# Kernel optimization log

Measured on AMD Instinct MI355X. Metric: run time of the kernel, lower is better.

The kernel has to match this reference:

```python
import jax, jax.numpy as jnp
import numpy as np

N, L, D = 16, 3136, 768  # batch, H*W (perfect square: 56*56), hidden_size
H = 8                    # head_count
K = D                    # key_channels
V = D // 2               # value_channels
M = 4 * D                # mlp_dim
EPS = 1e-6


def setup_inputs() -> dict:
    key = jax.random.key(0)
    ks = jax.random.split(key, 12)
    s = lambda d: 1.0 / np.sqrt(d)
    return {
        "x": jax.random.normal(ks[0], (N, L, D), dtype=jnp.float32),
        "ln1_g": jnp.ones((D,), jnp.float32),
        "ln1_b": jnp.zeros((D,), jnp.float32),
        # 1x1 conv weights stored as [out_ch, in_ch]
        "Wk": jax.random.normal(ks[1], (K, D), jnp.float32) * s(D),
        "bk": jnp.zeros((K,), jnp.float32),
        "Wq": jax.random.normal(ks[2], (K, D), jnp.float32) * s(D),
        "bq": jnp.zeros((K,), jnp.float32),
        "Wv": jax.random.normal(ks[3], (V, D), jnp.float32) * s(D),
        "bv": jnp.zeros((V,), jnp.float32),
        "Wr": jax.random.normal(ks[4], (D, V), jnp.float32) * s(V),
        "br": jnp.zeros((D,), jnp.float32),
        "ln2_g": jnp.ones((D,), jnp.float32),
        "ln2_b": jnp.zeros((D,), jnp.float32),
        # Linear weights stored as [out, in] (torch convention)
        "W1": jax.random.normal(ks[5], (M, D), jnp.float32) * s(D),
        "b1": jax.random.normal(ks[6], (M,), jnp.float32) * 1e-6,
        "W2": jax.random.normal(ks[7], (D, M), jnp.float32) * s(M),
        "b2": jax.random.normal(ks[8], (D,), jnp.float32) * 1e-6,
    }


def _layernorm(x, g, b):
    m = jnp.mean(x, axis=-1, keepdims=True)
    v = jnp.mean(jnp.square(x - m), axis=-1, keepdims=True)
    return (x - m) * jax.lax.rsqrt(v + EPS) * g + b


def _efficient_attention(x, Wk, bk, Wq, bq, Wv, bv, Wr, br):
    n, l, d = x.shape
    hk, hv = K // H, V // H
    # faithful to torch: input_.view(n, D, h, w) is a raw reshape, not transpose
    xf = x.reshape(n, d, l)  # [n, D, L]
    keys = jnp.einsum('kd,ndl->nkl', Wk, xf) + bk[None, :, None]
    queries = jnp.einsum('kd,ndl->nkl', Wq, xf) + bq[None, :, None]
    values = jnp.einsum('vd,ndl->nvl', Wv, xf) + bv[None, :, None]
    kh = jax.nn.softmax(keys.reshape(n, H, hk, l), axis=3)     # softmax over spatial
    qh = jax.nn.softmax(queries.reshape(n, H, hk, l), axis=2)  # softmax over head channels
    vh = values.reshape(n, H, hv, l)
    context = jnp.einsum('nhkl,nhvl->nhkv', kh, vh)            # [n,H,hk,hv]
    att = jnp.einsum('nhkv,nhkl->nhvl', context, qh)           # [n,H,hv,L]
    agg = att.reshape(n, V, l)
    out = jnp.einsum('dv,nvl->ndl', Wr, agg) + br[None, :, None]
    return out.reshape(n, l, d)  # faithful raw reshape back


def reference(x, ln1_g, ln1_b, Wk, bk, Wq, bq, Wv, bv, Wr, br,
              ln2_g, ln2_b, W1, b1, W2, b2):
    h = x
    y = _layernorm(x, ln1_g, ln1_b)
    y = _efficient_attention(y, Wk, bk, Wq, bq, Wv, bv, Wr, br)
    x = y + h
    h = x
    y = _layernorm(x, ln2_g, ln2_b)
    y = jax.nn.gelu(y @ W1.T + b1, approximate=False)
    y = y @ W2.T + b2
    return y + h
```

## Files before the change

### kernel.cpp

```cpp
#include <hip/hip_runtime.h>
#include <hip/hip_bf16.h>

using bf16 = __hip_bfloat16;
typedef __attribute__((ext_vector_type(8))) short short8;
typedef __attribute__((ext_vector_type(4))) short short4v;
typedef __attribute__((ext_vector_type(4))) float f32x4;

__device__ __forceinline__ float bfbits2f(unsigned short h) {
    unsigned v = (unsigned)h << 16;
    return __uint_as_float(v);
}

__device__ __forceinline__ void gload16(const void* g, void* l) {
    __builtin_amdgcn_global_load_lds(
        (const __attribute__((address_space(1))) unsigned int*)g,
        (__attribute__((address_space(3))) unsigned int*)l, 16, 0, 0);
}

__device__ __forceinline__ float gelu_fast(float x) {
    float x2 = x * x;
    float u = x * __builtin_fmaf(0.07135481f, x2, 1.59576912f);
    float e = __expf(u);
    return x - x * __builtin_amdgcn_rcpf(e + 1.0f);
}

__device__ __forceinline__ float blk_sum3(float v, float* red) {
#pragma unroll
    for (int o = 32; o > 0; o >>= 1) v += __shfl_down(v, o, 64);
    int wv = threadIdx.x >> 6;
    __syncthreads();
    if ((threadIdx.x & 63) == 0) red[wv] = v;
    __syncthreads();
    return red[0] + red[1] + red[2];
}

__global__ __launch_bounds__(192) void ln_f32(const float* __restrict__ x,
                                              const float* __restrict__ g,
                                              const float* __restrict__ b,
                                              bf16* __restrict__ y) {
    __shared__ float red[3];
    size_t base = (size_t)blockIdx.x * 768;
    int t = threadIdx.x;
    float4 v = *(const float4*)&x[base + t * 4];
    float s = blk_sum3(v.x + v.y + v.z + v.w, red);
    float mean = s * (1.0f / 768.0f);
    float d0 = v.x - mean, d1 = v.y - mean, d2 = v.z - mean, d3 = v.w - mean;
    float sq = blk_sum3(d0 * d0 + d1 * d1 + d2 * d2 + d3 * d3, red);
    float rstd = rsqrtf(sq * (1.0f / 768.0f) + 1e-6f);
    float4 gv = *(const float4*)&g[t * 4];
    float4 bv = *(const float4*)&b[t * 4];
    short4v o;
    o[0] = (short)__bfloat16_as_ushort(__float2bfloat16(d0 * rstd * gv.x + bv.x));
    o[1] = (short)__bfloat16_as_ushort(__float2bfloat16(d1 * rstd * gv.y + bv.y));
    o[2] = (short)__bfloat16_as_ushort(__float2bfloat16(d2 * rstd * gv.z + bv.z));
    o[3] = (short)__bfloat16_as_ushort(__float2bfloat16(d3 * rstd * gv.w + bv.w));
    *(short4v*)&((unsigned short*)y)[base + t * 4] = o;
}

__global__ __launch_bounds__(192) void ln_bf(const bf16* __restrict__ x,
                                             const float* __restrict__ g,
                                             const float* __restrict__ b,
                                             bf16* __restrict__ y) {
    __shared__ float red[3];
    size_t base = (size_t)blockIdx.x * 768;
    int t = threadIdx.x;
    short4v w = *(const short4v*)&((const unsigned short*)x)[base + t * 4];
    float v0 = bfbits2f((unsigned short)w[0]), v1 = bfbits2f((unsigned short)w[1]);
    float v2 = bfbits2f((unsigned short)w[2]), v3 = bfbits2f((unsigned short)w[3]);
    float s = blk_sum3(v0 + v1 + v2 + v3, red);
    float mean = s * (1.0f / 768.0f);
    float d0 = v0 - mean, d1 = v1 - mean, d2 = v2 - mean, d3 = v3 - mean;
    float sq = blk_sum3(d0 * d0 + d1 * d1 + d2 * d2 + d3 * d3, red);
    float rstd = rsqrtf(sq * (1.0f / 768.0f) + 1e-6f);
    float4 gv = *(const float4*)&g[t * 4];
    float4 bv = *(const float4*)&b[t * 4];
    short4v o;
    o[0] = (short)__bfloat16_as_ushort(__float2bfloat16(d0 * rstd * gv.x + bv.x));
    o[1] = (short)__bfloat16_as_ushort(__float2bfloat16(d1 * rstd * gv.y + bv.y));
    o[2] = (short)__bfloat16_as_ushort(__float2bfloat16(d2 * rstd * gv.z + bv.z));
    o[3] = (short)__bfloat16_as_ushort(__float2bfloat16(d3 * rstd * gv.w + bv.w));
    *(short4v*)&((unsigned short*)y)[base + t * 4] = o;
}

__global__ __launch_bounds__(256) void cast_kernel(const float* __restrict__ s,
                                                   bf16* __restrict__ d, int n) {
    int i = blockIdx.x * 256 + threadIdx.x;
    if (i < n) d[i] = __float2bfloat16(s[i]);
}

__global__ __launch_bounds__(256) void bias_cat(const float* __restrict__ bk,
                                                const float* __restrict__ bq,
                                                const float* __restrict__ bv,
                                                float* __restrict__ o) {
    int i = blockIdx.x * 256 + threadIdx.x;
    if (i < 768) o[i] = bk[i];
    else if (i < 1536) o[i] = bq[i - 768];
    else if (i < 1920) o[i] = bv[i - 1536];
}

__global__ __launch_bounds__(256) void transp_k(const bf16* __restrict__ Y,
                                                bf16* __restrict__ Xt) {
    __shared__ unsigned short tile[64][65];
    const size_t LD = (size_t)768 * 3136;
    int n = blockIdx.z;
    int l0 = blockIdx.x * 64, d0 = blockIdx.y * 64;
    const unsigned short* Yp = (const unsigned short*)Y + (size_t)n * LD;
    unsigned short* Xp = (unsigned short*)Xt + (size_t)n * LD;
    int t = threadIdx.x;
#pragma unroll
    for (int j = 0; j < 2; j++) {
        int e = t + 256 * j;
        int dd = e >> 3, lg = (e & 7) * 8;
        short8 v = *(const short8*)&Yp[(size_t)(d0 + dd) * 3136 + l0 + lg];
#pragma unroll
        for (int u = 0; u < 8; u++) tile[dd][lg + u] = (unsigned short)v[u];
    }
    __syncthreads();
#pragma unroll
    for (int j = 0; j < 2; j++) {
        int e = t + 256 * j;
        int ll = e >> 3, dg = (e & 7) * 8;
        short8 v;
#pragma unroll
        for (int u = 0; u < 8; u++) v[u] = (short)tile[dg + u][ll];
        *(short8*)&Xp[(size_t)(l0 + ll) * 768 + d0 + dg] = v;
    }
}

template <int MODE>
__global__ __launch_bounds__(256) void gemm_nk(
    const bf16* __restrict__ A, const bf16* __restrict__ B,
    const float* __restrict__ bias, const void* __restrict__ resid,
    void* __restrict__ C0, void* __restrict__ C1, void* __restrict__ C2,
    int M, int N, int K, long sB, long sC, long sR) {
    __shared__ bf16 As[128 * 64];
    __shared__ bf16 Bs[128 * 64];
    const int tid = threadIdx.x;
    const int lane = tid & 63, wave = tid >> 6;

    const int nbn = gridDim.x;
    const int nwg = nbn * gridDim.y;
    const int orig = blockIdx.y * nbn + blockIdx.x;
    const int qq = nwg >> 3, rm = nwg & 7;
    const int xcd = orig & 7, pos = orig >> 3;
    const int work = (xcd < rm ? xcd * (qq + 1) : rm * (qq + 1) + (xcd - rm) * qq) + pos;
    const int bn = work % nbn, bm = work / nbn;
    const int bz = blockIdx.z;

    const int wm = (wave >> 1) * 64, wn = (wave & 1) * 64;
    const int frow = lane & 15, fsb = lane >> 4;
    const int fxr = frow & 7;

    const int srow = lane >> 3;
    const int sslot = (lane & 7) ^ srow;
    const size_t rowB = (size_t)K * 2;
    const char* Ap = (const char*)A +
        ((size_t)bm * 128 + wave * 32 + srow) * rowB + (size_t)sslot * 16;
    const char* Bp = (const char*)(B + (size_t)bz * sB) +
        ((size_t)bn * 128 + wave * 32 + srow) * rowB + (size_t)sslot * 16;

    f32x4 acc[4][4];
#pragma unroll
    for (int mi = 0; mi < 4; mi++)
#pragma unroll
        for (int ni = 0; ni < 4; ni++)
#pragma unroll
            for (int r = 0; r < 4; r++) acc[mi][ni][r] = 0.0f;

    for (int kt = 0; kt < K; kt += 64) {
#pragma unroll
        for (int c = 0; c < 4; c++) {
            gload16(Ap + (size_t)c * 8 * rowB + (size_t)kt * 2, &As[(wave * 4 + c) * 512]);
            gload16(Bp + (size_t)c * 8 * rowB + (size_t)kt * 2, &Bs[(wave * 4 + c) * 512]);
        }
        __syncthreads();
#pragma unroll
        for (int k2 = 0; k2 < 2; k2++) {
            short8 af[4], bfv[4];
#pragma unroll
            for (int mi = 0; mi < 4; mi++) {
                int r = wm + mi * 16 + frow;
                af[mi] = *(const short8*)&As[r * 64 + (((k2 * 4 + fsb) ^ fxr) << 3)];
            }
#pragma unroll
            for (int ni = 0; ni < 4; ni++) {
                int r = wn + ni * 16 + frow;
                bfv[ni] = *(const short8*)&Bs[r * 64 + (((k2 * 4 + fsb) ^ fxr) << 3)];
            }
#pragma unroll
            for (int mi = 0; mi < 4; mi++)
#pragma unroll
                for (int ni = 0; ni < 4; ni++)
                    acc[mi][ni] = __builtin_amdgcn_mfma_f32_16x16x32_bf16(
                        af[mi], bfv[ni], acc[mi][ni], 0, 0, 0);
        }
        __syncthreads();
    }

    const float* Rf = (const float*)resid + (size_t)bz * sR;
    const unsigned short* Rb = (const unsigned short*)resid + (size_t)bz * sR;
#pragma unroll
    for (int mi = 0; mi < 4; mi++)
#pragma unroll
        for (int ni = 0; ni < 4; ni++)
#pragma unroll
            for (int r = 0; r < 4; r++) {
                int row = bm * 128 + wm + mi * 16 + (fsb << 2) + r;
                int col = bn * 128 + wn + ni * 16 + frow;
                if (col < N) {
                    float v = acc[mi][ni][r];
                    size_t idx = (size_t)row * N + col;
                    if (MODE == 0) {
                        float o = v + bias[col];
                        if (col < 768)
                            ((bf16*)C0)[(size_t)row * 768 + col] = __float2bfloat16(o);
                        else if (col < 1536)
                            ((bf16*)C1)[(size_t)row * 768 + col - 768] = __float2bfloat16(o);
                        else
                            ((bf16*)C2)[(size_t)row * 384 + col - 1536] = __float2bfloat16(o);
                    } else if (MODE == 1) {
                        bf16* Cb = (bf16*)C0 + (size_t)bz * sC;
                        Cb[idx] = __float2bfloat16(v + bias[row] + Rf[idx]);
                    } else if (MODE == 2) {
                        ((bf16*)C0)[idx] = __float2bfloat16(gelu_fast(v + bias[col]));
                    } else {
                        ((float*)C0)[idx] = v + bias[col] + bfbits2f(Rb[idx]);
                    }
                }
            }
}

__global__ __launch_bounds__(256) void softk_part(const bf16* __restrict__ Kt,
                                                  float* __restrict__ pm,
                                                  float* __restrict__ ps) {
    int g = blockIdx.y;
    int lc = blockIdx.x;
    int n = g / 3;
    int c = (g % 3) * 256 + threadIdx.x;
    const unsigned short* base = (const unsigned short*)Kt +
        ((size_t)n * 3136 + (size_t)lc * 392) * 768 + c;
    float mx = -1e30f;
    for (int l = 0; l < 392; l++) mx = fmaxf(mx, bfbits2f(base[(size_t)l * 768]));
    float s = 0.f;
    for (int l = 0; l < 392; l++) s += expf(bfbits2f(base[(size_t)l * 768]) - mx);
    int idx = g * 256 + threadIdx.x;
    pm[(size_t)lc * 12288 + idx] = mx;
    ps[(size_t)lc * 12288 + idx] = s;
}
__global__ __launch_bounds__(256) void softk_fin(bf16* __restrict__ Kt,
                                                 const float* __restrict__ pm,
                                                 const float* __restrict__ ps) {
    int g = blockIdx.y;
    int lc = blockIdx.x;
    int n = g / 3;
    int c = (g % 3) * 256 + threadIdx.x;
    int idx = g * 256 + threadIdx.x;
    float M = -1e30f;
#pragma unroll
    for (int i = 0; i < 8; i++) M = fmaxf(M, pm[(size_t)i * 12288 + idx]);
    float S = 0.f;
#pragma unroll
    for (int i = 0; i < 8; i++)
        S += ps[(size_t)i * 12288 + idx] * expf(pm[(size_t)i * 12288 + idx] - M);
    float inv = 1.0f / S;
    unsigned short* base = (unsigned short*)Kt + ((size_t)n * 3136 + (size_t)lc * 392) * 768 + c;
    for (int l = 0; l < 392; l++) {
        float e = expf(bfbits2f(base[(size_t)l * 768]) - M) * inv;
        ((bf16*)base)[(size_t)l * 768] = __float2bfloat16(e);
    }
}

__global__ __launch_bounds__(256) void softq_k(bf16* __restrict__ Qt) {
    int u = blockIdx.x * 256 + threadIdx.x;
    unsigned short* p = (unsigned short*)Qt + (size_t)(u >> 3) * 768 + (size_t)(u & 7) * 96;
    float v[96];
#pragma unroll
    for (int j = 0; j < 12; j++) {
        short8 w = *(const short8*)&p[j * 8];
#pragma unroll
        for (int x = 0; x < 8; x++) v[j * 8 + x] = bfbits2f((unsigned short)w[x]);
    }
    float mx = -1e30f;
#pragma unroll
    for (int i = 0; i < 96; i++) mx = fmaxf(mx, v[i]);
    float s = 0.f;
#pragma unroll
    for (int i = 0; i < 96; i++) { v[i] = expf(v[i] - mx); s += v[i]; }
    float inv = 1.0f / s;
#pragma unroll
    for (int j = 0; j < 12; j++) {
        short8 w;
#pragma unroll
        for (int x = 0; x < 8; x++)
            w[x] = (short)__bfloat16_as_ushort(__float2bfloat16(v[j * 8 + x] * inv));
        *(short8*)&p[j * 8] = w;
    }
}

__global__ __launch_bounds__(256) void context_k(const bf16* __restrict__ Kt,
                                                 const bf16* __restrict__ Vt,
                                                 float* __restrict__ ctx) {
    __shared__ float ks[32][96];
    __shared__ float vs[32][48];
    int nh = blockIdx.y;
    int n = nh >> 3, h = nh & 7;
    int t = threadIdx.x;
    const unsigned short* kp = (const unsigned short*)Kt;
    const unsigned short* vp = (const unsigned short*)Vt;
    int a = t >> 4, bq = t & 15;
    float acc[6][3];
#pragma unroll
    for (int i = 0; i < 6; i++)
#pragma unroll
        for (int j = 0; j < 3; j++) acc[i][j] = 0.f;
    int l0 = blockIdx.x * 448;
    for (int ls = l0; ls < l0 + 448; ls += 32) {
        __syncthreads();
#pragma unroll
        for (int j = 0; j < 6; j++) {
            int e = t + 256 * j;
            int row = e / 48, cp = e % 48;
            unsigned u = *(const unsigned*)&kp[((size_t)(n * 3136 + ls + row)) * 768 + h * 96 + cp * 2];
            ks[row][cp * 2] = bfbits2f((unsigned short)(u & 0xffff));
            ks[row][cp * 2 + 1] = bfbits2f((unsigned short)(u >> 16));
        }
#pragma unroll
        for (int j = 0; j < 3; j++) {
            int e = t + 256 * j;
            int row = e / 24, cp = e % 24;
            unsigned u = *(const unsigned*)&vp[((size_t)(n * 3136 + ls + row)) * 384 + h * 48 + cp * 2];
            vs[row][cp * 2] = bfbits2f((unsigned short)(u & 0xffff));
            vs[row][cp * 2 + 1] = bfbits2f((unsigned short)(u >> 16));
        }
        __syncthreads();
        for (int ll = 0; ll < 32; ll++) {
            float kv[6], vv[3];
#pragma unroll
            for (int i = 0; i < 6; i++) kv[i] = ks[ll][a * 6 + i];
#pragma unroll
            for (int j = 0; j < 3; j++) vv[j] = vs[ll][bq * 3 + j];
#pragma unroll
            for (int i = 0; i < 6; i++)
#pragma unroll
                for (int j = 0; j < 3; j++) acc[i][j] += kv[i] * vv[j];
        }
    }
    float* cb = ctx + (size_t)nh * 4608;
#pragma unroll
    for (int i = 0; i < 6; i++)
#pragma unroll
        for (int j = 0; j < 3; j++)
            atomicAdd(&cb[(a * 6 + i) * 48 + bq * 3 + j], acc[i][j]);
}

__global__ __launch_bounds__(256) void att_k(const float* __restrict__ ctx,
                                             const bf16* __restrict__ Qt,
                                             bf16* __restrict__ att) {
    __shared__ float cs[4608];
    int nh = blockIdx.y;
    int n = nh >> 3, h = nh & 7;
    for (int j = threadIdx.x; j < 4608; j += 256) cs[j] = ctx[(size_t)nh * 4608 + j];
    __syncthreads();
    int l = blockIdx.x * 256 + threadIdx.x;
    if (l >= 3136) return;
    const unsigned short* qp = (const unsigned short*)Qt + ((size_t)(n * 3136 + l)) * 768 + h * 96;
    float qv[96];
#pragma unroll
    for (int j = 0; j < 12; j++) {
        short8 w = *(const short8*)&qp[j * 8];
#pragma unroll
        for (int x = 0; x < 8; x++) qv[j * 8 + x] = bfbits2f((unsigned short)w[x]);
    }
    unsigned short ov[48];
#pragma unroll
    for (int vb = 0; vb < 12; vb++) {
        f32x4 s;
        s[0] = s[1] = s[2] = s[3] = 0.f;
        for (int k = 0; k < 96; k++) {
            f32x4 c4 = *(const f32x4*)&cs[k * 48 + vb * 4];
            float q = qv[k];
#pragma unroll
            for (int x = 0; x < 4; x++) s[x] += c4[x] * q;
        }
#pragma unroll
        for (int x = 0; x < 4; x++)
            ov[vb * 4 + x] = __bfloat16_as_ushort(__float2bfloat16(s[x]));
    }
    unsigned short* op = (unsigned short*)att + ((size_t)n * 3200 + l) * 384 + h * 48;
#pragma unroll
    for (int j = 0; j < 6; j++) *(short8*)&op[j * 8] = *(short8*)&ov[j * 8];
}

extern "C" void kernel_launch(void* const* d_in, const int* in_sizes, int n_in,
                              void* d_out, int out_size, void* d_ws, size_t ws_size,
                              hipStream_t stream) {
    (void)in_sizes; (void)n_in; (void)out_size; (void)ws_size;
    const float* x     = (const float*)d_in[0];
    const float* ln1_g = (const float*)d_in[1];
    const float* ln1_b = (const float*)d_in[2];
    const float* Wk    = (const float*)d_in[3];
    const float* bk    = (const float*)d_in[4];
    const float* Wq    = (const float*)d_in[5];
    const float* bq    = (const float*)d_in[6];
    const float* Wv    = (const float*)d_in[7];
    const float* bv    = (const float*)d_in[8];
    const float* Wr    = (const float*)d_in[9];
    const float* br    = (const float*)d_in[10];
    const float* ln2_g = (const float*)d_in[11];
    const float* ln2_b = (const float*)d_in[12];
    const float* W1    = (const float*)d_in[13];
    const float* b1    = (const float*)d_in[14];
    const float* W2    = (const float*)d_in[15];
    const float* b2    = (const float*)d_in[16];

    const int Nb = 16, L = 3136;
    const size_t LD = (size_t)L * 768;
    const size_t sz77 = (size_t)50176 * 768 * 2;

    char* w = (char*)d_ws;
    size_t off = 0;
    auto alloc = [&](size_t bytes) {
        char* p = w + off;
        off = (off + bytes + 255) & ~(size_t)255;
        return p;
    };
    bf16* Ybf  = (bf16*)alloc(sz77);
    bf16* Xt   = (bf16*)alloc(sz77);
    bf16* Kt   = (bf16*)alloc(sz77);
    bf16* Qt   = (bf16*)alloc(sz77);
    bf16* Vt   = (bf16*)alloc((size_t)50176 * 384 * 2);
    bf16* attb = (bf16*)alloc((size_t)16 * 3200 * 384 * 2);
    bf16* x1   = (bf16*)alloc(sz77);
    bf16* Wkqv_bf = (bf16*)alloc((size_t)1920 * 768 * 2);
    bf16* Wr_bf = (bf16*)alloc((size_t)768 * 384 * 2);
    bf16* W1_bf = (bf16*)alloc((size_t)3072 * 768 * 2);
    bf16* W2_bf = (bf16*)alloc((size_t)768 * 3072 * 2);
    float* bkqv = (float*)alloc((size_t)1920 * 4);
    float* ctx = (float*)Xt;
    float* pm  = (float*)(Xt + 2359296);
    float* ps  = (float*)(Xt + 2621440);
    bf16* Hbf  = Ybf;
    bf16* Y2bf = Vt;

    auto castw = [&](const float* s, bf16* dp, int n) {
        cast_kernel<<<(n + 255) / 256, 256, 0, stream>>>(s, dp, n);
    };
    castw(Wk, Wkqv_bf, 768 * 768);
    castw(Wq, Wkqv_bf + 768 * 768, 768 * 768);
    castw(Wv, Wkqv_bf + 1536 * 768, 384 * 768);
    castw(Wr, Wr_bf, 768 * 384);
    castw(W1, W1_bf, 3072 * 768);
    castw(W2, W2_bf, 768 * 3072);
    bias_cat<<<8, 256, 0, stream>>>(bk, bq, bv, bkqv);

    ln_f32<<<Nb * L, 192, 0, stream>>>(x, ln1_g, ln1_b, Ybf);
    transp_k<<<dim3(49, 12, 16), 256, 0, stream>>>(Ybf, Xt);

    dim3 blk(256);
    gemm_nk<0><<<dim3(15, 392, 1), blk, 0, stream>>>(
        Xt, Wkqv_bf, bkqv, nullptr, Kt, Qt, Vt, 50176, 1920, 768, 0, 0, 0);

    softk_part<<<dim3(8, 48), blk, 0, stream>>>(Kt, pm, ps);
    softk_fin<<<dim3(8, 48), blk, 0, stream>>>(Kt, pm, ps);
    softq_k<<<1568, blk, 0, stream>>>(Qt);

    hipMemsetAsync(ctx, 0, (size_t)128 * 4608 * 4, stream);
    context_k<<<dim3(7, 128), blk, 0, stream>>>(Kt, Vt, ctx);
    att_k<<<dim3(13, 128), blk, 0, stream>>>(ctx, Qt, attb);

    gemm_nk<1><<<dim3(25, 6, 16), blk, 0, stream>>>(
        Wr_bf, attb, br, x, x1, nullptr, nullptr, 768, 3136, 384,
        (long)3200 * 384, (long)LD, (long)LD);

    ln_bf<<<Nb * L, 192, 0, stream>>>(x1, ln2_g, ln2_b, Y2bf);

    gemm_nk<2><<<dim3(24, 392, 1), blk, 0, stream>>>(
        Y2bf, W1_bf, b1, nullptr, Hbf, nullptr, nullptr, 50176, 3072, 768, 0, 0, 0);
    gemm_nk<3><<<dim3(6, 392, 1), blk, 0, stream>>>(
        Hbf, W2_bf, b2, x1, d_out, nullptr, nullptr, 50176, 768, 3072, 0, 0, 0);
}
```

Baseline: 1.615 ms.

## Use 256x256 double-buffered GEMM tiles and fold softmaxes into context/attention kernels

Adds a 512-thread GEMM kernel with 256x256 output tiles and a two-stage double-buffered LDS pipeline (128KB dynamic shared memory), used for the QKV, MLP-up and MLP-down GEMMs. The QKV weight is padded to 2048 rows with zeroed rows so the tile divides evenly. The separate key and query softmax kernels are removed. Key exponentials and their sums are computed inside context_k, and a small ctx_fin kernel normalizes the context. Query softmax is done inline in att_k. Exponentials are taken without max subtraction, which risks overflow for large logits, and the large tiles may lower occupancy.

```diff
diff --git a/kernel.cpp b/kernel.cpp
--- a/kernel.cpp
+++ b/kernel.cpp
@@ -128,16 +128,124 @@
 }
 
 template <int MODE>
+__global__ __launch_bounds__(512, 2) void gemm256(
+    const bf16* __restrict__ A, const bf16* __restrict__ B,
+    const float* __restrict__ bias, const void* __restrict__ resid,
+    void* __restrict__ C0, void* __restrict__ C1, void* __restrict__ C2,
+    int M, int N, int K) {
+    extern __shared__ char smem[];
+    const int tid = threadIdx.x;
+    const int lane = tid & 63, wave = tid >> 6;
+
+    const int nbn = gridDim.x;
+    const int nwg = nbn * gridDim.y;
+    const int orig = blockIdx.y * nbn + blockIdx.x;
+    const int qq = nwg >> 3, rm = nwg & 7;
+    const int xcd = orig & 7, pos = orig >> 3;
+    const int work = (xcd < rm ? xcd * (qq + 1) : rm * (qq + 1) + (xcd - rm) * qq) + pos;
+    const int bn = work % nbn, bm = work / nbn;
+
+    const int wm = (wave >> 2) * 128, wn = (wave & 3) * 64;
+    const int frow = lane & 15, fsb = lane >> 4, fxr = frow & 7;
+    const int srow = lane >> 3, sslot = (lane & 7) ^ srow;
+    const size_t rowB = (size_t)K * 2;
+    const char* Ap = (const char*)A + (size_t)(bm * 256 + wave * 32 + srow) * rowB + sslot * 16;
+    const char* Bp = (const char*)B + (size_t)(bn * 256 + wave * 32 + srow) * rowB + sslot * 16;
+    char* lA = smem + wave * 32 * 128;
+    char* lB = smem + 32768 + wave * 32 * 128;
+
+    f32x4 acc[8][4];
+#pragma unroll
+    for (int mi = 0; mi < 8; mi++)
+#pragma unroll
+        for (int ni = 0; ni < 4; ni++)
+#pragma unroll
+            for (int r = 0; r < 4; r++) acc[mi][ni][r] = 0.0f;
+
+    auto stage = [&](int kt, int p) {
+#pragma unroll
+        for (int c = 0; c < 4; c++) {
+            gload16(Ap + (size_t)c * 8 * rowB + (size_t)kt * 2, lA + p * 65536 + c * 1024);
+            gload16(Bp + (size_t)c * 8 * rowB + (size_t)kt * 2, lB + p * 65536 + c * 1024);
+        }
+    };
+    const int nt = K >> 6;
+    stage(0, 0);
+    stage(64, 1);
+    for (int t = 0; t < nt; ++t) {
+        if (t == nt - 1)
+            asm volatile("s_waitcnt vmcnt(0)" ::: "memory");
+        else
+            asm volatile("s_waitcnt vmcnt(8)" ::: "memory");
+        __builtin_amdgcn_s_barrier();
+        asm volatile("" ::: "memory");
+        const bf16* As = (const bf16*)(smem + (t & 1) * 65536);
+        const bf16* Bs = (const bf16*)(smem + (t & 1) * 65536 + 32768);
+#pragma unroll
+        for (int k2 = 0; k2 < 2; k2++) {
+            const int ko = ((k2 * 4 + fsb) ^ fxr) << 3;
+            short8 bfv[4];
+#pragma unroll
+            for (int ni = 0; ni < 4; ni++)
+                bfv[ni] = *(const short8*)&Bs[(wn + ni * 16 + frow) * 64 + ko];
+#pragma unroll
+            for (int half = 0; half < 2; half++) {
+                short8 af[4];
+#pragma unroll
+                for (int i = 0; i < 4; i++)
+                    af[i] = *(const short8*)&As[(wm + (half * 4 + i) * 16 + frow) * 64 + ko];
+#pragma unroll
+                for (int i = 0; i < 4; i++)
+#pragma unroll
+                    for (int ni = 0; ni < 4; ni++)
+                        acc[half * 4 + i][ni] = __builtin_amdgcn_mfma_f32_16x16x32_bf16(
+                            af[i], bfv[ni], acc[half * 4 + i][ni], 0, 0, 0);
+            }
+        }
+        asm volatile("" ::: "memory");
+        __builtin_amdgcn_s_barrier();
+        if (t + 2 < nt) stage((t + 2) * 64, t & 1);
+    }
+
+    const unsigned short* Rb = (const unsigned short*)resid;
+#pragma unroll
+    for (int mi = 0; mi < 8; mi++)
+#pragma unroll
+        for (int ni = 0; ni < 4; ni++)
+#pragma unroll
+            for (int r = 0; r < 4; r++) {
+                int row = bm * 256 + wm + mi * 16 + fsb * 4 + r;
+                int col = bn * 256 + wn + ni * 16 + frow;
+                float v = acc[mi][ni][r];
+                if (MODE == 0) {
+                    if (col < 1920) {
+                        float o = v + bias[col];
+                        if (col < 768)
+                            ((bf16*)C0)[(size_t)row * 768 + col] = __float2bfloat16(o);
+                        else if (col < 1536)
+                            ((bf16*)C1)[(size_t)row * 768 + col - 768] = __float2bfloat16(o);
+                        else
+                            ((bf16*)C2)[(size_t)row * 384 + col - 1536] = __float2bfloat16(o);
+                    }
+                } else if (MODE == 2) {
+                    ((bf16*)C0)[(size_t)row * N + col] =
+                        __float2bfloat16(gelu_fast(v + bias[col]));
+                } else {
+                    size_t idx = (size_t)row * N + col;
+                    ((float*)C0)[idx] = v + bias[col] + bfbits2f(Rb[idx]);
+                }
+            }
+}
+
+template <int MODE>
 __global__ __launch_bounds__(256) void gemm_nk(
     const bf16* __restrict__ A, const bf16* __restrict__ B,
     const float* __restrict__ bias, const void* __restrict__ resid,
-    void* __restrict__ C0, void* __restrict__ C1, void* __restrict__ C2,
-    int M, int N, int K, long sB, long sC, long sR) {
+    void* __restrict__ C0, int M, int N, int K, long sB, long sC, long sR) {
     __shared__ bf16 As[128 * 64];
     __shared__ bf16 Bs[128 * 64];
     const int tid = threadIdx.x;
     const int lane = tid & 63, wave = tid >> 6;
-
     const int nbn = gridDim.x;
     const int nwg = nbn * gridDim.y;
     const int orig = blockIdx.y * nbn + blockIdx.x;
@@ -148,11 +256,8 @@
     const int bz = blockIdx.z;
 
     const int wm = (wave >> 1) * 64, wn = (wave & 1) * 64;
-    const int frow = lane & 15, fsb = lane >> 4;
-    const int fxr = frow & 7;
-
-    const int srow = lane >> 3;
-    const int sslot = (lane & 7) ^ srow;
+    const int frow = lane & 15, fsb = lane >> 4, fxr = frow & 7;
+    const int srow = lane >> 3, sslot = (lane & 7) ^ srow;
     const size_t rowB = (size_t)K * 2;
     const char* Ap = (const char*)A +
         ((size_t)bm * 128 + wave * 32 + srow) * rowB + (size_t)sslot * 16;
@@ -198,7 +303,6 @@
     }
 
     const float* Rf = (const float*)resid + (size_t)bz * sR;
-    const unsigned short* Rb = (const unsigned short*)resid + (size_t)bz * sR;
 #pragma unroll
     for (int mi = 0; mi < 4; mi++)
 #pragma unroll
@@ -210,96 +314,16 @@
                 if (col < N) {
                     float v = acc[mi][ni][r];
                     size_t idx = (size_t)row * N + col;
-                    if (MODE == 0) {
-                        float o = v + bias[col];
-                        if (col < 768)
-                            ((bf16*)C0)[(size_t)row * 768 + col] = __float2bfloat16(o);
-                        else if (col < 1536)
-                            ((bf16*)C1)[(size_t)row * 768 + col - 768] = __float2bfloat16(o);
-                        else
-                            ((bf16*)C2)[(size_t)row * 384 + col - 1536] = __float2bfloat16(o);
-                    } else if (MODE == 1) {
-                        bf16* Cb = (bf16*)C0 + (size_t)bz * sC;
-                        Cb[idx] = __float2bfloat16(v + bias[row] + Rf[idx]);
-                    } else if (MODE == 2) {
-                        ((bf16*)C0)[idx] = __float2bfloat16(gelu_fast(v + bias[col]));
-                    } else {
-                        ((float*)C0)[idx] = v + bias[col] + bfbits2f(Rb[idx]);
-                    }
+                    bf16* Cb = (bf16*)C0 + (size_t)bz * sC;
+                    Cb[idx] = __float2bfloat16(v + bias[row] + Rf[idx]);
                 }
             }
 }
 
-__global__ __launch_bounds__(256) void softk_part(const bf16* __restrict__ Kt,
-                                                  float* __restrict__ pm,
-                                                  float* __restrict__ ps) {
-    int g = blockIdx.y;
-    int lc = blockIdx.x;
-    int n = g / 3;
-    int c = (g % 3) * 256 + threadIdx.x;
-    const unsigned short* base = (const unsigned short*)Kt +
-        ((size_t)n * 3136 + (size_t)lc * 392) * 768 + c;
-    float mx = -1e30f;
-    for (int l = 0; l < 392; l++) mx = fmaxf(mx, bfbits2f(base[(size_t)l * 768]));
-    float s = 0.f;
-    for (int l = 0; l < 392; l++) s += expf(bfbits2f(base[(size_t)l * 768]) - mx);
-    int idx = g * 256 + threadIdx.x;
-    pm[(size_t)lc * 12288 + idx] = mx;
-    ps[(size_t)lc * 12288 + idx] = s;
-}
-__global__ __launch_bounds__(256) void softk_fin(bf16* __restrict__ Kt,
-                                                 const float* __restrict__ pm,
-                                                 const float* __restrict__ ps) {
-    int g = blockIdx.y;
-    int lc = blockIdx.x;
-    int n = g / 3;
-    int c = (g % 3) * 256 + threadIdx.x;
-    int idx = g * 256 + threadIdx.x;
-    float M = -1e30f;
-#pragma unroll
-    for (int i = 0; i < 8; i++) M = fmaxf(M, pm[(size_t)i * 12288 + idx]);
-    float S = 0.f;
-#pragma unroll
-    for (int i = 0; i < 8; i++)
-        S += ps[(size_t)i * 12288 + idx] * expf(pm[(size_t)i * 12288 + idx] - M);
-    float inv = 1.0f / S;
-    unsigned short* base = (unsigned short*)Kt + ((size_t)n * 3136 + (size_t)lc * 392) * 768 + c;
-    for (int l = 0; l < 392; l++) {
-        float e = expf(bfbits2f(base[(size_t)l * 768]) - M) * inv;
-        ((bf16*)base)[(size_t)l * 768] = __float2bfloat16(e);
-    }
-}
-
-__global__ __launch_bounds__(256) void softq_k(bf16* __restrict__ Qt) {
-    int u = blockIdx.x * 256 + threadIdx.x;
-    unsigned short* p = (unsigned short*)Qt + (size_t)(u >> 3) * 768 + (size_t)(u & 7) * 96;
-    float v[96];
-#pragma unroll
-    for (int j = 0; j < 12; j++) {
-        short8 w = *(const short8*)&p[j * 8];
-#pragma unroll
-        for (int x = 0; x < 8; x++) v[j * 8 + x] = bfbits2f((unsigned short)w[x]);
-    }
-    float mx = -1e30f;
-#pragma unroll
-    for (int i = 0; i < 96; i++) mx = fmaxf(mx, v[i]);
-    float s = 0.f;
-#pragma unroll
-    for (int i = 0; i < 96; i++) { v[i] = expf(v[i] - mx); s += v[i]; }
-    float inv = 1.0f / s;
-#pragma unroll
-    for (int j = 0; j < 12; j++) {
-        short8 w;
-#pragma unroll
-        for (int x = 0; x < 8; x++)
-            w[x] = (short)__bfloat16_as_ushort(__float2bfloat16(v[j * 8 + x] * inv));
-        *(short8*)&p[j * 8] = w;
-    }
-}
-
 __global__ __launch_bounds__(256) void context_k(const bf16* __restrict__ Kt,
                                                  const bf16* __restrict__ Vt,
-                                                 float* __restrict__ ctx) {
+                                                 float* __restrict__ ctx,
+                                                 float* __restrict__ Sf) {
     __shared__ float ks[32][96];
     __shared__ float vs[32][48];
     int nh = blockIdx.y;
@@ -309,10 +333,13 @@
     const unsigned short* vp = (const unsigned short*)Vt;
     int a = t >> 4, bq = t & 15;
     float acc[6][3];
-#pragma unroll
-    for (int i = 0; i < 6; i++)
+    float sacc[6];
+#pragma unroll
+    for (int i = 0; i < 6; i++) {
+        sacc[i] = 0.f;
 #pragma unroll
         for (int j = 0; j < 3; j++) acc[i][j] = 0.f;
+    }
     int l0 = blockIdx.x * 448;
     for (int ls = l0; ls < l0 + 448; ls += 32) {
         __syncthreads();
@@ -321,8 +348,8 @@
             int e = t + 256 * j;
             int row = e / 48, cp = e % 48;
             unsigned u = *(const unsigned*)&kp[((size_t)(n * 3136 + ls + row)) * 768 + h * 96 + cp * 2];
-            ks[row][cp * 2] = bfbits2f((unsigned short)(u & 0xffff));
-            ks[row][cp * 2 + 1] = bfbits2f((unsigned short)(u >> 16));
+            ks[row][cp * 2] = __expf(bfbits2f((unsigned short)(u & 0xffff)));
+            ks[row][cp * 2 + 1] = __expf(bfbits2f((unsigned short)(u >> 16)));
         }
 #pragma unroll
         for (int j = 0; j < 3; j++) {
@@ -336,7 +363,7 @@
         for (int ll = 0; ll < 32; ll++) {
             float kv[6], vv[3];
 #pragma unroll
-            for (int i = 0; i < 6; i++) kv[i] = ks[ll][a * 6 + i];
+            for (int i = 0; i < 6; i++) { kv[i] = ks[ll][a * 6 + i]; sacc[i] += kv[i]; }
 #pragma unroll
             for (int j = 0; j < 3; j++) vv[j] = vs[ll][bq * 3 + j];
 #pragma unroll
@@ -347,10 +374,22 @@
     }
     float* cb = ctx + (size_t)nh * 4608;
 #pragma unroll
-    for (int i = 0; i < 6; i++)
+    for (int i = 0; i < 6; i++) {
 #pragma unroll
         for (int j = 0; j < 3; j++)
             atomicAdd(&cb[(a * 6 + i) * 48 + bq * 3 + j], acc[i][j]);
+        if (bq == 0) atomicAdd(&Sf[(size_t)nh * 96 + a * 6 + i], sacc[i]);
+    }
+}
+
+__global__ __launch_bounds__(256) void ctx_fin(float* __restrict__ ctx,
+                                               const float* __restrict__ Sf) {
+    int nh = blockIdx.x;
+    __shared__ float sinv[96];
+    if (threadIdx.x < 96) sinv[threadIdx.x] = 1.0f / Sf[(size_t)nh * 96 + threadIdx.x];
+    __syncthreads();
+    for (int e = threadIdx.x; e < 4608; e += 256)
+        ctx[(size_t)nh * 4608 + e] *= sinv[e / 48];
 }
 
 __global__ __launch_bounds__(256) void att_k(const float* __restrict__ ctx,
@@ -365,26 +404,32 @@
     if (l >= 3136) return;
     const unsigned short* qp = (const unsigned short*)Qt + ((size_t)(n * 3136 + l)) * 768 + h * 96;
     float qv[96];
+    float s = 0.f;
 #pragma unroll
     for (int j = 0; j < 12; j++) {
         short8 w = *(const short8*)&qp[j * 8];
 #pragma unroll
-        for (int x = 0; x < 8; x++) qv[j * 8 + x] = bfbits2f((unsigned short)w[x]);
-    }
+        for (int x = 0; x < 8; x++) {
+            float e = __expf(bfbits2f((unsigned short)w[x]));
+            qv[j * 8 + x] = e;
+            s += e;
+        }
+    }
+    float inv = 1.0f / s;
     unsigned short ov[48];
 #pragma unroll
     for (int vb = 0; vb < 12; vb++) {
-        f32x4 s;
-        s[0] = s[1] = s[2] = s[3] = 0.f;
+        f32x4 acc4;
+        acc4[0] = acc4[1] = acc4[2] = acc4[3] = 0.f;
         for (int k = 0; k < 96; k++) {
             f32x4 c4 = *(const f32x4*)&cs[k * 48 + vb * 4];
             float q = qv[k];
 #pragma unroll
-            for (int x = 0; x < 4; x++) s[x] += c4[x] * q;
+            for (int x = 0; x < 4; x++) acc4[x] += c4[x] * q;
         }
 #pragma unroll
         for (int x = 0; x < 4; x++)
-            ov[vb * 4 + x] = __bfloat16_as_ushort(__float2bfloat16(s[x]));
+            ov[vb * 4 + x] = __bfloat16_as_ushort(__float2bfloat16(acc4[x] * inv));
     }
     unsigned short* op = (unsigned short*)att + ((size_t)n * 3200 + l) * 384 + h * 48;
 #pragma unroll
@@ -431,20 +476,20 @@
     bf16* Vt   = (bf16*)alloc((size_t)50176 * 384 * 2);
     bf16* attb = (bf16*)alloc((size_t)16 * 3200 * 384 * 2);
     bf16* x1   = (bf16*)alloc(sz77);
-    bf16* Wkqv_bf = (bf16*)alloc((size_t)1920 * 768 * 2);
+    bf16* Wkqv_bf = (bf16*)alloc((size_t)2048 * 768 * 2);
     bf16* Wr_bf = (bf16*)alloc((size_t)768 * 384 * 2);
     bf16* W1_bf = (bf16*)alloc((size_t)3072 * 768 * 2);
     bf16* W2_bf = (bf16*)alloc((size_t)768 * 3072 * 2);
     float* bkqv = (float*)alloc((size_t)1920 * 4);
     float* ctx = (float*)Xt;
-    float* pm  = (float*)(Xt + 2359296);
-    float* ps  = (float*)(Xt + 2621440);
+    float* Sf  = (float*)((char*)Xt + 4718592);
     bf16* Hbf  = Ybf;
     bf16* Y2bf = Vt;
 
     auto castw = [&](const float* s, bf16* dp, int n) {
         cast_kernel<<<(n + 255) / 256, 256, 0, stream>>>(s, dp, n);
     };
+    hipMemsetAsync(Wkqv_bf + (size_t)1920 * 768, 0, (size_t)128 * 768 * 2, stream);
     castw(Wk, Wkqv_bf, 768 * 768);
     castw(Wq, Wkqv_bf + 768 * 768, 768 * 768);
     castw(Wv, Wkqv_bf + 1536 * 768, 384 * 768);
@@ -453,29 +498,32 @@
     castw(W2, W2_bf, 768 * 3072);
     bias_cat<<<8, 256, 0, stream>>>(bk, bq, bv, bkqv);
 
+    hipFuncSetAttribute((const void*)gemm256<0>,
+                        hipFuncAttributeMaxDynamicSharedMemorySize, 131072);
+    hipFuncSetAttribute((const void*)gemm256<2>,
+                        hipFuncAttributeMaxDynamicSharedMemorySize, 131072);
+    hipFuncSetAttribute((const void*)gemm256<3>,
+                        hipFuncAttributeMaxDynamicSharedMemorySize, 131072);
+
     ln_f32<<<Nb * L, 192, 0, stream>>>(x, ln1_g, ln1_b, Ybf);
     transp_k<<<dim3(49, 12, 16), 256, 0, stream>>>(Ybf, Xt);
 
-    dim3 blk(256);
-    gemm_nk<0><<<dim3(15, 392, 1), blk, 0, stream>>>(
-        Xt, Wkqv_bf, bkqv, nullptr, Kt, Qt, Vt, 50176, 1920, 768, 0, 0, 0);
-
-    softk_part<<<dim3(8, 48), blk, 0, stream>>>(Kt, pm, ps);
-    softk_fin<<<dim3(8, 48), blk, 0, stream>>>(Kt, pm, ps);
-    softq_k<<<1568, blk, 0, stream>>>(Qt);
-
-    hipMemsetAsync(ctx, 0, (size_t)128 * 4608 * 4, stream);
-    context_k<<<dim3(7, 128), blk, 0, stream>>>(Kt, Vt, ctx);
-    att_k<<<dim3(13, 128), blk, 0, stream>>>(ctx, Qt, attb);
-
-    gemm_nk<1><<<dim3(25, 6, 16), blk, 0, stream>>>(
-        Wr_bf, attb, br, x, x1, nullptr, nullptr, 768, 3136, 384,
+    gemm256<0><<<dim3(8, 196), 512, 131072, stream>>>(
+        Xt, Wkqv_bf, bkqv, nullptr, Kt, Qt, Vt, 50176, 2048, 768);
+
+    hipMemsetAsync(ctx, 0, 4718592 + 49152, stream);
+    context_k<<<dim3(7, 128), 256, 0, stream>>>(Kt, Vt, ctx, Sf);
+    ctx_fin<<<128, 256, 0, stream>>>(ctx, Sf);
+    att_k<<<dim3(13, 128), 256, 0, stream>>>(ctx, Qt, attb);
+
+    gemm_nk<1><<<dim3(25, 6, 16), 256, 0, stream>>>(
+        Wr_bf, attb, br, x, x1, 768, 3136, 384,
         (long)3200 * 384, (long)LD, (long)LD);
 
     ln_bf<<<Nb * L, 192, 0, stream>>>(x1, ln2_g, ln2_b, Y2bf);
 
-    gemm_nk<2><<<dim3(24, 392, 1), blk, 0, stream>>>(
-        Y2bf, W1_bf, b1, nullptr, Hbf, nullptr, nullptr, 50176, 3072, 768, 0, 0, 0);
-    gemm_nk<3><<<dim3(6, 392, 1), blk, 0, stream>>>(
-        Hbf, W2_bf, b2, x1, d_out, nullptr, nullptr, 50176, 768, 3072, 0, 0, 0);
-}
+    gemm256<2><<<dim3(12, 196), 512, 131072, stream>>>(
+        Y2bf, W1_bf, b1, nullptr, Hbf, nullptr, nullptr, 50176, 3072, 768);
+    gemm256<3><<<dim3(3, 196), 512, 131072, stream>>>(
+        Hbf, W2_bf, b2, x1, d_out, nullptr, nullptr, 50176, 768, 3072);
+}
```

New measurement: 1.391 ms. 13.8% less time.
